# Kernel tuning notes

Measured on AMD Instinct MI355X. Metric: run time of the kernel, lower is better.

## Reference

```python
import jax, jax.numpy as jnp
import numpy as np

B, T = 64, 2048
D_RNN, D_EMB, D_ATT = 1024, 512, 128
N_FILT, KSIZE = 32, 31
PAD = (KSIZE - 1) // 2


def setup_inputs() -> dict:
    key = jax.random.key(0)
    ks = jax.random.split(key, 9)
    return {
        "attention_hidden_state": jax.random.normal(ks[0], (B, D_RNN), jnp.float32),
        "memory": jax.random.normal(ks[1], (B, T, D_EMB), jnp.float32),
        "processed_memory": jax.random.normal(ks[2], (B, T, D_ATT), jnp.float32),
        "attention_weights_cat": jax.random.uniform(ks[3], (B, 2, T), jnp.float32),
        "mask": jax.random.randint(ks[4], (B, T), 0, 2) > 0,
        # learned params (all bias-free, as in the torch module)
        "Wq": jax.random.normal(ks[5], (D_ATT, D_RNN), jnp.float32) * 0.02,   # query_layer.weight
        "Wv": jax.random.normal(ks[6], (1, D_ATT), jnp.float32) * 0.02,        # v.weight
        "conv_w": jax.random.normal(ks[7], (N_FILT, 2, KSIZE), jnp.float32) * 0.1,  # location_conv.weight (OIH)
        "Wd": jax.random.normal(ks[8], (D_ATT, N_FILT), jnp.float32) * 0.02,   # location_dense.weight
    }


def reference(attention_hidden_state, memory, processed_memory,
              attention_weights_cat, mask, Wq, Wv, conv_w, Wd):
    # processed query: [B, 1, D_ATT]
    pq = (attention_hidden_state @ Wq.T)[:, None, :]
    # location features: Conv1d(2 -> N_FILT, same padding) over time
    loc = jax.lax.conv_general_dilated(
        attention_weights_cat, conv_w,
        window_strides=(1,), padding=[(PAD, PAD)],
        dimension_numbers=("NCH", "OIH", "NCH"))           # [B, N_FILT, T]
    paw = jnp.einsum("bft,af->bta", loc, Wd)               # [B, T, D_ATT]
    # additive energies -> scalar per position via v-projection
    energies = jnp.einsum("bta,a->bt", jnp.tanh(pq + paw + processed_memory), Wv[0])
    alignment = jnp.where(mask, -jnp.inf, energies)         # masked fill
    attention_weights = jax.nn.softmax(alignment, axis=1)   # [B, T]
    attention_context = jnp.einsum("bt,btd->bd", attention_weights, memory)  # [B, D_EMB]
    return attention_context, jax.lax.stop_gradient(attention_weights)
```

## Files before the change

kernel.cpp:

```cpp
#include <hip/hip_runtime.h>
#include <math.h>

#define B_    64
#define T_    2048
#define DRNN  1024
#define DEMB  512
#define DATT  128
#define NF    32
#define KS    31
#define PADL  15
#define MP    64
#define TT    32

__device__ __forceinline__ float fast_tanh(float x){
    float e2 = __expf(2.0f * x);
    return 1.0f - 2.0f / (e2 + 1.0f);
}

__global__ __launch_bounds__(128) void prep_kernel(
    const float* __restrict__ hidden, const float* __restrict__ Wq,
    const float* __restrict__ Wd, const float* __restrict__ convw,
    float* __restrict__ pq, float* __restrict__ M)
{
    const int blk = blockIdx.x;
    const int a = threadIdx.x;
    if (blk < B_) {
        __shared__ float sh[DRNN];
        const int b = blk;
        #pragma unroll
        for (int i = 0; i < DRNN/128; ++i) sh[a + 128*i] = hidden[b*DRNN + a + 128*i];
        __syncthreads();
        const float4* wq4 = (const float4*)(Wq + a*DRNN);
        float acc = 0.f;
        #pragma unroll 4
        for (int k = 0; k < DRNN/4; ++k){
            float4 w = wq4[k];
            acc = fmaf(w.x, sh[4*k+0], acc);
            acc = fmaf(w.y, sh[4*k+1], acc);
            acc = fmaf(w.z, sh[4*k+2], acc);
            acc = fmaf(w.w, sh[4*k+3], acc);
        }
        pq[b*DATT + a] = acc;
    } else {
        float wd[NF];
        #pragma unroll
        for (int f = 0; f < NF; ++f) wd[f] = Wd[a*NF + f];
        for (int ck = 0; ck < 2*KS; ++ck){
            float acc = 0.f;
            #pragma unroll
            for (int f = 0; f < NF; ++f) acc = fmaf(wd[f], convw[f*2*KS + ck], acc);
            M[a*MP + ck] = acc;
        }
    }
}

__global__ __launch_bounds__(256) void energy_kernel(
    const float* __restrict__ pm, const float* __restrict__ awcat,
    const float* __restrict__ pq, const float* __restrict__ M,
    const float* __restrict__ Wv, const int* __restrict__ mask,
    float* __restrict__ ev, float* __restrict__ pmax, float* __restrict__ psum)
{
    const int b   = blockIdx.y;
    const int t0  = blockIdx.x * 64;
    const int tid = threadIdx.x;
    const int s   = tid >> 7;
    const int a   = tid & 127;
    const int ts  = t0 + TT * s;

    __shared__ float saw0[96], saw1[96];
    __shared__ float sred[2][2][TT];

    for (int i = tid; i < 94; i += 256){
        int tt = t0 - PADL + i;
        bool ok = (tt >= 0) && (tt < T_);
        saw0[i] = ok ? awcat[(b*2+0)*T_ + tt] : 0.f;
        saw1[i] = ok ? awcat[(b*2+1)*T_ + tt] : 0.f;
    }
    __syncthreads();

    float Ma0[KS], Ma1[KS];
    const float* Mrow = M + a*MP;
    #pragma unroll
    for (int k = 0; k < KS; ++k){ Ma0[k] = Mrow[k]; Ma1[k] = Mrow[KS + k]; }
    const float pqa = pq[b*DATT + a];
    const float wv  = Wv[a];

    float acc[TT];
    #pragma unroll
    for (int t = 0; t < TT; ++t) acc[t] = pqa;

    #pragma unroll
    for (int j = 0; j < TT + KS - 1; ++j){
        const float av0 = saw0[j + TT*s];
        const float av1 = saw1[j + TT*s];
        const int tlo = (j - KS + 1) > 0 ? (j - KS + 1) : 0;
        const int thi = (j < TT - 1) ? j : (TT - 1);
        #pragma unroll
        for (int t = tlo; t <= thi; ++t){
            acc[t] = fmaf(Ma0[j - t], av0, acc[t]);
            acc[t] = fmaf(Ma1[j - t], av1, acc[t]);
        }
    }

    const float* pmb = pm + ((size_t)(b*T_ + ts)) * DATT + a;
    #pragma unroll
    for (int t = 0; t < TT; ++t){
        float x = acc[t] + pmb[(size_t)t * DATT];
        acc[t] = wv * fast_tanh(x);
    }

    const int lane = tid & 63;
    const int half = a >> 6;
    #pragma unroll
    for (int t = 0; t < TT; ++t){
        float r = acc[t];
        r += __shfl_xor(r, 1, 64);  r += __shfl_xor(r, 2, 64);
        r += __shfl_xor(r, 4, 64);  r += __shfl_xor(r, 8, 64);
        r += __shfl_xor(r, 16, 64); r += __shfl_xor(r, 32, 64);
        if (lane == 0) sred[s][half][t] = r;
    }
    __syncthreads();

    if (tid < 64){
        const int tile = tid >> 5, tl = tid & 31;
        const int t = t0 + tid;
        float e = sred[tile][0][tl] + sred[tile][1][tl];
        const int mk = mask[b*T_ + t];
        if (mk) e = -INFINITY;
        ev[b*T_ + t] = e;
        float mval = mk ? -1e30f : e;
        #pragma unroll
        for (int off = 1; off < 64; off <<= 1) mval = fmaxf(mval, __shfl_xor(mval, off, 64));
        float sv = mk ? 0.f : __expf(e - mval);
        #pragma unroll
        for (int off = 1; off < 64; off <<= 1) sv += __shfl_xor(sv, off, 64);
        if (tid == 0){
            pmax[b*32 + blockIdx.x] = mval;
            psum[b*32 + blockIdx.x] = sv;
        }
    }
}

__global__ __launch_bounds__(256) void context_kernel(
    const float* __restrict__ ev, const float* __restrict__ pmax,
    const float* __restrict__ psum, const float* __restrict__ memory,
    float* __restrict__ ctx, float* __restrict__ wout)
{
    const int b   = blockIdx.y;
    const int t0  = blockIdx.x * 256;
    const int tid = threadIdx.x;
    __shared__ float sw[256];
    __shared__ float sstat[2];
    __shared__ float4 sacc[128];

    if (tid < 64){
        float pmv = (tid < 32) ? pmax[b*32 + tid] : -1e30f;
        float psv = (tid < 32) ? psum[b*32 + tid] : 0.f;
        float g = pmv;
        #pragma unroll
        for (int off = 1; off < 64; off <<= 1) g = fmaxf(g, __shfl_xor(g, off, 64));
        float c = psv * __expf(pmv - g);
        #pragma unroll
        for (int off = 1; off < 64; off <<= 1) c += __shfl_xor(c, off, 64);
        if (tid == 0){ sstat[0] = g; sstat[1] = 1.0f / c; }
    }
    __syncthreads();
    const float gmax = sstat[0], rinv = sstat[1];
    {
        const int t = t0 + tid;
        const float e = ev[b*T_ + t];
        const float w = __expf(e - gmax) * rinv;
        sw[tid] = w;
        wout[b*T_ + t] = w;
    }
    __syncthreads();

    const int col = tid & 127;
    const int row = tid >> 7;
    float4 acc = make_float4(0.f, 0.f, 0.f, 0.f);
    const float4* mem4 = (const float4*)memory + ((size_t)(b*T_ + t0))*(DEMB/4) + col;
    #pragma unroll 8
    for (int tt = row; tt < 256; tt += 2){
        const float w = sw[tt];
        const float4 m = mem4[(size_t)tt * (DEMB/4)];
        acc.x = fmaf(w, m.x, acc.x);
        acc.y = fmaf(w, m.y, acc.y);
        acc.z = fmaf(w, m.z, acc.z);
        acc.w = fmaf(w, m.w, acc.w);
    }
    if (row == 1) sacc[col] = acc;
    __syncthreads();
    if (row == 0){
        const float4 o = sacc[col];
        atomicAdd(&ctx[b*DEMB + 4*col + 0], acc.x + o.x);
        atomicAdd(&ctx[b*DEMB + 4*col + 1], acc.y + o.y);
        atomicAdd(&ctx[b*DEMB + 4*col + 2], acc.z + o.z);
        atomicAdd(&ctx[b*DEMB + 4*col + 3], acc.w + o.w);
    }
}

extern "C" void kernel_launch(void* const* d_in, const int* in_sizes, int n_in,
                              void* d_out, int out_size, void* d_ws, size_t ws_size,
                              hipStream_t stream)
{
    const float* hidden = (const float*)d_in[0];
    const float* memory = (const float*)d_in[1];
    const float* pm     = (const float*)d_in[2];
    const float* awcat  = (const float*)d_in[3];
    const int*   mask   = (const int*)d_in[4];
    const float* Wq     = (const float*)d_in[5];
    const float* Wv     = (const float*)d_in[6];
    const float* convw  = (const float*)d_in[7];
    const float* Wd     = (const float*)d_in[8];

    float* out  = (float*)d_out;
    float* ctx  = out;
    float* wout = out + B_*DEMB;

    float* pq    = (float*)d_ws;
    float* M     = pq + B_*DATT;
    float* ev    = M + DATT*MP;
    float* pmax  = ev + B_*T_;
    float* psum  = pmax + B_*32;

    hipMemsetAsync(ctx, 0, B_*DEMB*sizeof(float), stream);

    prep_kernel<<<dim3(B_ + 1), 128, 0, stream>>>(hidden, Wq, Wd, convw, pq, M);
    energy_kernel<<<dim3(T_/64, B_), 256, 0, stream>>>(pm, awcat, pq, M, Wv, mask, ev, pmax, psum);
    context_kernel<<<dim3(T_/256, B_), 256, 0, stream>>>(ev, pmax, psum, memory, ctx, wout);
}
```

Baseline: 488.8 us.

## Fuse energy and context passes with split-softmax partial contexts per chunk

Merges the energy and context kernels into one: each 64-step chunk computes local softmax numerators and a locally weighted partial context over memory, writing per-chunk partials. A small finalize kernel rescales the partials with the global max and sum, and writes the final weights. This removes the energy round trip, the memset and the atomics, and skips memory rows where the weight is zero (masked positions). In exchange it adds a partial-context buffer of B*32*512 floats and a serial 32-chunk reduction per batch.

```diff
diff --git a/kernel.cpp b/kernel.cpp
--- a/kernel.cpp
+++ b/kernel.cpp
@@ -11,6 +11,8 @@
 #define PADL  15
 #define MP    64
 #define TT    32
+#define CT    64
+#define NC    (T_/CT)
 
 __device__ __forceinline__ float fast_tanh(float x){
     float e2 = __expf(2.0f * x);
@@ -54,14 +56,17 @@
     }
 }
 
-__global__ __launch_bounds__(256) void energy_kernel(
+__global__ __launch_bounds__(256) void fused_kernel(
     const float* __restrict__ pm, const float* __restrict__ awcat,
     const float* __restrict__ pq, const float* __restrict__ M,
     const float* __restrict__ Wv, const int* __restrict__ mask,
-    float* __restrict__ ev, float* __restrict__ pmax, float* __restrict__ psum)
+    const float* __restrict__ memory,
+    float* __restrict__ pbuf, float* __restrict__ pmax,
+    float* __restrict__ psum, float* __restrict__ pctx)
 {
     const int b   = blockIdx.y;
-    const int t0  = blockIdx.x * 64;
+    const int cx  = blockIdx.x;
+    const int t0  = cx * CT;
     const int tid = threadIdx.x;
     const int s   = tid >> 7;
     const int a   = tid & 127;
@@ -69,6 +74,8 @@
 
     __shared__ float saw0[96], saw1[96];
     __shared__ float sred[2][2][TT];
+    __shared__ float sp[CT];
+    __shared__ float4 sacc[128];
 
     for (int i = tid; i < 94; i += 256){
         int tt = t0 - PADL + i;
@@ -122,80 +129,87 @@
     __syncthreads();
 
     if (tid < 64){
-        const int tile = tid >> 5, tl = tid & 31;
         const int t = t0 + tid;
-        float e = sred[tile][0][tl] + sred[tile][1][tl];
+        float e = sred[tid>>5][0][tid&31] + sred[tid>>5][1][tid&31];
         const int mk = mask[b*T_ + t];
-        if (mk) e = -INFINITY;
-        ev[b*T_ + t] = e;
         float mval = mk ? -1e30f : e;
         #pragma unroll
         for (int off = 1; off < 64; off <<= 1) mval = fmaxf(mval, __shfl_xor(mval, off, 64));
-        float sv = mk ? 0.f : __expf(e - mval);
+        const float pval = mk ? 0.f : __expf(e - mval);
+        float sv = pval;
         #pragma unroll
         for (int off = 1; off < 64; off <<= 1) sv += __shfl_xor(sv, off, 64);
+        sp[tid] = pval;
+        pbuf[b*T_ + t] = pval;
         if (tid == 0){
-            pmax[b*32 + blockIdx.x] = mval;
-            psum[b*32 + blockIdx.x] = sv;
-        }
-    }
-}
-
-__global__ __launch_bounds__(256) void context_kernel(
-    const float* __restrict__ ev, const float* __restrict__ pmax,
-    const float* __restrict__ psum, const float* __restrict__ memory,
-    float* __restrict__ ctx, float* __restrict__ wout)
-{
-    const int b   = blockIdx.y;
-    const int t0  = blockIdx.x * 256;
-    const int tid = threadIdx.x;
-    __shared__ float sw[256];
-    __shared__ float sstat[2];
-    __shared__ float4 sacc[128];
-
-    if (tid < 64){
-        float pmv = (tid < 32) ? pmax[b*32 + tid] : -1e30f;
-        float psv = (tid < 32) ? psum[b*32 + tid] : 0.f;
-        float g = pmv;
-        #pragma unroll
-        for (int off = 1; off < 64; off <<= 1) g = fmaxf(g, __shfl_xor(g, off, 64));
-        float c = psv * __expf(pmv - g);
-        #pragma unroll
-        for (int off = 1; off < 64; off <<= 1) c += __shfl_xor(c, off, 64);
-        if (tid == 0){ sstat[0] = g; sstat[1] = 1.0f / c; }
-    }
-    __syncthreads();
-    const float gmax = sstat[0], rinv = sstat[1];
-    {
-        const int t = t0 + tid;
-        const float e = ev[b*T_ + t];
-        const float w = __expf(e - gmax) * rinv;
-        sw[tid] = w;
-        wout[b*T_ + t] = w;
+            pmax[b*NC + cx] = mval;
+            psum[b*NC + cx] = sv;
+        }
     }
     __syncthreads();
 
     const int col = tid & 127;
     const int row = tid >> 7;
-    float4 acc = make_float4(0.f, 0.f, 0.f, 0.f);
+    float4 a4 = make_float4(0.f, 0.f, 0.f, 0.f);
     const float4* mem4 = (const float4*)memory + ((size_t)(b*T_ + t0))*(DEMB/4) + col;
-    #pragma unroll 8
-    for (int tt = row; tt < 256; tt += 2){
-        const float w = sw[tt];
-        const float4 m = mem4[(size_t)tt * (DEMB/4)];
-        acc.x = fmaf(w, m.x, acc.x);
-        acc.y = fmaf(w, m.y, acc.y);
-        acc.z = fmaf(w, m.z, acc.z);
-        acc.w = fmaf(w, m.w, acc.w);
-    }
-    if (row == 1) sacc[col] = acc;
+    for (int tt = row; tt < CT; tt += 2){
+        const float w = sp[tt];
+        if (w != 0.f){
+            const float4 m = mem4[(size_t)tt * (DEMB/4)];
+            a4.x = fmaf(w, m.x, a4.x);
+            a4.y = fmaf(w, m.y, a4.y);
+            a4.z = fmaf(w, m.z, a4.z);
+            a4.w = fmaf(w, m.w, a4.w);
+        }
+    }
+    if (row == 1) sacc[col] = a4;
     __syncthreads();
     if (row == 0){
         const float4 o = sacc[col];
-        atomicAdd(&ctx[b*DEMB + 4*col + 0], acc.x + o.x);
-        atomicAdd(&ctx[b*DEMB + 4*col + 1], acc.y + o.y);
-        atomicAdd(&ctx[b*DEMB + 4*col + 2], acc.z + o.z);
-        atomicAdd(&ctx[b*DEMB + 4*col + 3], acc.w + o.w);
+        float4* dst = (float4*)(pctx + ((size_t)(b*NC + cx))*DEMB) + col;
+        *dst = make_float4(a4.x + o.x, a4.y + o.y, a4.z + o.z, a4.w + o.w);
+    }
+}
+
+__global__ __launch_bounds__(256) void finalize_kernel(
+    const float* __restrict__ pbuf, const float* __restrict__ pmax,
+    const float* __restrict__ psum, const float* __restrict__ pctx,
+    float* __restrict__ ctx, float* __restrict__ wout)
+{
+    const int b = blockIdx.x;
+    const int tid = threadIdx.x;
+    __shared__ float sscale[NC];
+
+    if (tid < 64){
+        float mv = (tid < NC) ? pmax[b*NC + tid] : -1e30f;
+        float sv = (tid < NC) ? psum[b*NC + tid] : 0.f;
+        float g = mv;
+        #pragma unroll
+        for (int off = 1; off < 64; off <<= 1) g = fmaxf(g, __shfl_xor(g, off, 64));
+        float z = sv * __expf(mv - g);
+        #pragma unroll
+        for (int off = 1; off < 64; off <<= 1) z += __shfl_xor(z, off, 64);
+        if (tid < NC) sscale[tid] = __expf(mv - g) / z;
+    }
+    __syncthreads();
+
+    float2 a2 = make_float2(0.f, 0.f);
+    const float2* pc2 = (const float2*)(pctx + (size_t)b*NC*DEMB) + tid;
+    #pragma unroll
+    for (int c = 0; c < NC; ++c){
+        const float sc = sscale[c];
+        if (sc != 0.f){
+            const float2 v = pc2[(size_t)c * (DEMB/2)];
+            a2.x = fmaf(sc, v.x, a2.x);
+            a2.y = fmaf(sc, v.y, a2.y);
+        }
+    }
+    ((float2*)(ctx + b*DEMB))[tid] = a2;
+
+    #pragma unroll
+    for (int i = 0; i < T_/256; ++i){
+        const int t = tid + 256*i;
+        wout[b*T_ + t] = pbuf[b*T_ + t] * sscale[t >> 6];
     }
 }
 
@@ -218,14 +232,14 @@
     float* wout = out + B_*DEMB;
 
     float* pq    = (float*)d_ws;
-    float* M     = pq + B_*DATT;
-    float* ev    = M + DATT*MP;
-    float* pmax  = ev + B_*T_;
-    float* psum  = pmax + B_*32;
-
-    hipMemsetAsync(ctx, 0, B_*DEMB*sizeof(float), stream);
+    float* M     = pq   + B_*DATT;
+    float* pbuf  = M    + DATT*MP;
+    float* pmax  = pbuf + B_*T_;
+    float* psum  = pmax + B_*NC;
+    float* pctx  = psum + B_*NC;
 
     prep_kernel<<<dim3(B_ + 1), 128, 0, stream>>>(hidden, Wq, Wd, convw, pq, M);
-    energy_kernel<<<dim3(T_/64, B_), 256, 0, stream>>>(pm, awcat, pq, M, Wv, mask, ev, pmax, psum);
-    context_kernel<<<dim3(T_/256, B_), 256, 0, stream>>>(ev, pmax, psum, memory, ctx, wout);
-}
+    fused_kernel<<<dim3(NC, B_), 256, 0, stream>>>(pm, awcat, pq, M, Wv, mask,
+                                                   memory, pbuf, pmax, psum, pctx);
+    finalize_kernel<<<dim3(B_), 256, 0, stream>>>(pbuf, pmax, psum, pctx, ctx, wout);
+}
```

New measurement: 484.2 us. About the same (-0.9%).
